# Kernel tuning notes

Measured on AMD Instinct MI355X. Metric: run time of the kernel, lower is better.

## Reference

```python
import jax, jax.numpy as jnp
import numpy as np

S = 60            # voxel grid side
N = 100000        # active voxels
M_PAD = 60000     # padded pairs per kernel offset
C_IN = 64
C_OUT = 64
KV = 27           # kernel volume (3^3)
CENTER = 13


def _build_maps():
    rng = np.random.default_rng(0)
    lin = rng.choice(S ** 3, size=N, replace=False)
    coords = np.stack(np.unravel_index(lin, (S, S, S)), axis=1).astype(np.int64)  # [N,3]
    lut = -np.ones(S ** 3, dtype=np.int64)
    lut[lin] = np.arange(N)
    imap = -np.ones((KV - 1, M_PAD), dtype=np.int32)
    omap = -np.ones((KV - 1, M_PAD), dtype=np.int32)
    row = 0
    for k in range(KV):
        if k == CENTER:
            continue
        d = np.array([k // 9 - 1, (k // 3) % 3 - 1, k % 3 - 1])
        nb = coords + d
        valid = np.all((nb >= 0) & (nb < S), axis=1)
        linnb = nb[:, 0] * S * S + nb[:, 1] * S + nb[:, 2]
        j = np.where(valid, lut[np.clip(linnb, 0, S ** 3 - 1)], -1)
        mask = j >= 0
        src = np.nonzero(mask)[0].astype(np.int32)   # input idx (gather)
        dst = j[mask].astype(np.int32)               # output idx (scatter)
        m = min(src.shape[0], M_PAD)
        imap[row, :m] = src[:m]
        omap[row, :m] = dst[:m]
        row += 1
    return imap, omap


def setup_inputs() -> dict:
    key = jax.random.key(0)
    kf, kw = jax.random.split(key)
    feats = jax.random.normal(kf, (N, C_IN), dtype=jnp.float32)
    stdv = 1.0 / np.sqrt(C_OUT * KV)
    kernel = jax.random.uniform(kw, (KV, C_IN, C_OUT), dtype=jnp.float32,
                                minval=-stdv, maxval=stdv)
    imap_np, omap_np = _build_maps()
    return {
        "feats": feats,
        "kernel": kernel,
        "imap": jnp.asarray(imap_np),
        "omap": jnp.asarray(omap_np),
    }


def reference(feats, kernel, imap, omap):
    # Submanifold sparse 3D conv: center weight applied densely,
    # 26 neighbor offsets via gather -> per-offset GEMM -> scatter-add.
    # feats: [N, Cin], kernel: [27, Cin, Cout], imap/omap: [26, M] (-1 = pad)
    koff = jnp.concatenate([jnp.arange(CENTER), jnp.arange(CENTER + 1, KV)])
    w_off = kernel[koff]                                   # [26, Cin, Cout]
    out = feats @ kernel[CENTER]                           # [N, Cout] center GEMM
    valid = (imap >= 0)                                    # [26, M]
    gathered = feats[jnp.clip(imap, 0)] * valid[..., None].astype(feats.dtype)  # [26, M, Cin]
    partial = jnp.einsum('kmc,kco->kmo', gathered, w_off)  # [26, M, Cout]
    dst = jnp.where(valid, omap, 0).reshape(-1)            # padded rows contribute zeros
    out = out.at[dst].add(partial.reshape(-1, partial.shape[-1]))
    return out
```

## Files before the change

### kernel.cpp

```cpp
#include <hip/hip_runtime.h>


#define N_PTS 100000
#define MPAD  60000
#define C     64
#define NSL   27

typedef short bf16x8 __attribute__((ext_vector_type(8)));
typedef float f32x4  __attribute__((ext_vector_type(4)));

static __device__ inline unsigned short f2bf(float x) {
    unsigned int u = __float_as_uint(x);
    u += 0x7fffu + ((u >> 16) & 1u);
    return (unsigned short)(u >> 16);
}

#define FEATS16_BYTES ((size_t)(N_PTS + 1) * C * 2)
#define WFRAG_OFF     (((FEATS16_BYTES) + 255) & ~(size_t)255)
#define WFRAG_BYTES   ((size_t)NSL * 8192)
#define NBR_OFF       (WFRAG_OFF + WFRAG_BYTES)
#define NBR_BYTES     ((size_t)26 * N_PTS * 4)

#define FEAT_ITEMS 800008
#define WF_ITEMS   (NSL * 2 * 4 * 64)
#define SCAT_ITEMS (26 * MPAD / 4)
#define PREP_TOTAL (FEAT_ITEMS + WF_ITEMS + SCAT_ITEMS)

__global__ __launch_bounds__(256) void prep_one(const float* __restrict__ feats,
                                                const float* __restrict__ kern,
                                                const int* __restrict__ imap,
                                                const int* __restrict__ omap,
                                                unsigned short* __restrict__ f16,
                                                unsigned short* __restrict__ wf,
                                                int* __restrict__ nbr) {
    const int idx = blockIdx.x * 256 + threadIdx.x;
    if (idx < FEAT_ITEMS) {
        bf16x8* dst = (bf16x8*)f16;
        if (idx < FEAT_ITEMS - 8) {
            const float4* src = (const float4*)feats;
            const float4 a = src[2 * idx];
            const float4 b = src[2 * idx + 1];
            bf16x8 v;
            v[0] = (short)f2bf(a.x); v[1] = (short)f2bf(a.y);
            v[2] = (short)f2bf(a.z); v[3] = (short)f2bf(a.w);
            v[4] = (short)f2bf(b.x); v[5] = (short)f2bf(b.y);
            v[6] = (short)f2bf(b.z); v[7] = (short)f2bf(b.w);
            dst[idx] = v;
        } else {
            dst[idx] = (bf16x8){0, 0, 0, 0, 0, 0, 0, 0};
        }
    } else if (idx < FEAT_ITEMS + WF_ITEMS) {
        const int w = idx - FEAT_ITEMS;
        const int lane = w & 63;
        const int rest = w >> 6;
        const int ct = rest & 3;
        const int kk = (rest >> 2) & 1;
        const int s  = rest >> 3;
        bf16x8 v = (bf16x8){0, 0, 0, 0, 0, 0, 0, 0};
        if (s < NSL) {
            const int q = lane >> 4, t = lane & 15;
            const int ksrc = (s == 26) ? 13 : (s + (s >= 13 ? 1 : 0));
            const int k0 = kk * 32 + q * 8;
            const int n  = ct * 16 + t;
            const float* wp = kern + (size_t)ksrc * 4096 + n;
            #pragma unroll
            for (int j = 0; j < 8; ++j) v[j] = (short)f2bf(wp[(size_t)(k0 + j) * 64]);
        }
        ((bf16x8*)wf)[w] = v;
    } else {
        const int k = idx - (FEAT_ITEMS + WF_ITEMS);
        if (k < SCAT_ITEMS) {
            const int s = k / (MPAD / 4);
            const int v = k - s * (MPAD / 4);
            const int4 iv = ((const int4*)(imap + (size_t)s * MPAD))[v];
            const int4 ov = ((const int4*)(omap + (size_t)s * MPAD))[v];
            int* nb = nbr + (size_t)s * N_PTS;
            if (iv.x >= 0) nb[ov.x] = iv.x;
            if (iv.y >= 0) nb[ov.y] = iv.y;
            if (iv.z >= 0) nb[ov.z] = iv.z;
            if (iv.w >= 0) nb[ov.w] = iv.w;
        }
    }
}

static __device__ inline void gl_lds(const char* g, char* l) {
    __builtin_amdgcn_global_load_lds(
        (const __attribute__((address_space(1))) unsigned int*)g,
        (__attribute__((address_space(3))) unsigned int*)l, 16, 0, 0);
}

#define WAITV(n) asm volatile("s_waitcnt vmcnt(" #n ")" ::: "memory")
#define FENCE    asm volatile("" ::: "memory")

__global__ __launch_bounds__(256, 4) void spconv_main(const unsigned short* __restrict__ f16,
                                                      const unsigned short* __restrict__ wf,
                                                      const int* __restrict__ nbr,
                                                      float* __restrict__ out) {
    __shared__ __align__(16) char bsm[3][8192];

    const int lane = threadIdx.x & 63;
    const int wave = threadIdx.x >> 6;
    const int q = lane >> 4, t = lane & 15;
    const int R0 = blockIdx.x * 64 + wave * 16;
    const int row = R0 + t;
    const bool inb = (row < N_PTS);
    const int safe = inb ? row : 0;

    const bf16x8* fv = (const bf16x8*)f16;
    const char* wfb  = (const char*)wf;

    int jr[3];
    bf16x8 Ar[3][2];

#define LOADJ(s_)  do { jr[(s_) % 3] = nbr[(size_t)(s_) * N_PTS + safe]; } while (0)

#define GATHER(s_) do { \
        int j_ = ((s_) == 26) ? (inb ? row : -1) : (inb ? jr[(s_) % 3] : -1); \
        const int jz = ((unsigned)j_ < (unsigned)N_PTS) ? j_ : N_PTS; \
        const bf16x8* ap = fv + (size_t)jz * 8; \
        Ar[(s_) % 3][0] = ap[q]; \
        Ar[(s_) % 3][1] = ap[4 + q]; \
    } while (0)

#define STAGEB(s_) do { \
        const char* gs = wfb + (size_t)(s_) * 8192 + wave * 2048 + lane * 16; \
        char* bd = (char*)bsm[(s_) % 3] + wave * 2048; \
        gl_lds(gs, bd); gl_lds(gs + 1024, bd + 1024); \
    } while (0)

    LOADJ(0); LOADJ(1); FENCE;
    STAGEB(0); FENCE; GATHER(0); FENCE; LOADJ(2); FENCE;
    STAGEB(1); FENCE; GATHER(1); FENCE; LOADJ(3); FENCE;
    WAITV(8);
    __builtin_amdgcn_s_barrier();
    FENCE;

    f32x4 acc[4];
    #pragma unroll
    for (int c = 0; c < 4; ++c) acc[c] = (f32x4){0.f, 0.f, 0.f, 0.f};

    #pragma unroll
    for (int s = 0; s < NSL; ++s) {
        if (s + 2 <= 26) { STAGEB(s + 2); FENCE; GATHER(s + 2); FENCE; }
        if (s + 4 <= 25) { LOADJ(s + 4); FENCE; }

        const char* bb = (const char*)bsm[s % 3];
        bf16x8 B0[4], B1[4];
        #pragma unroll
        for (int ct = 0; ct < 4; ++ct) {
            B0[ct] = *(const bf16x8*)(bb +        ct * 1024 + lane * 16);
            B1[ct] = *(const bf16x8*)(bb + 4096 + ct * 1024 + lane * 16);
        }
        __builtin_amdgcn_s_setprio(1);
        #pragma unroll
        for (int ct = 0; ct < 4; ++ct)
            acc[ct] = __builtin_amdgcn_mfma_f32_16x16x32_bf16(Ar[s % 3][0], B0[ct], acc[ct], 0, 0, 0);
        #pragma unroll
        for (int ct = 0; ct < 4; ++ct)
            acc[ct] = __builtin_amdgcn_mfma_f32_16x16x32_bf16(Ar[s % 3][1], B1[ct], acc[ct], 0, 0, 0);
        __builtin_amdgcn_s_setprio(0);

        if (s < 26) {
            if (s <= 21)      WAITV(8);
            else if (s == 22) WAITV(7);
            else if (s <= 24) WAITV(6);
            else              WAITV(2);
            __builtin_amdgcn_s_barrier();
            FENCE;
        }
    }

#undef LOADJ
#undef GATHER
#undef STAGEB

    #pragma unroll
    for (int i = 0; i < 4; ++i) {
        const int r = R0 + 4 * q + i;
        if (r < N_PTS) {
            #pragma unroll
            for (int ct = 0; ct < 4; ++ct)
                out[(size_t)r * C + ct * 16 + t] = acc[ct][i];
        }
    }
}

extern "C" void kernel_launch(void* const* d_in, const int* in_sizes, int n_in,
                              void* d_out, int out_size, void* d_ws, size_t ws_size,
                              hipStream_t stream) {
    const float* feats = (const float*)d_in[0];
    const float* kern  = (const float*)d_in[1];
    const int*   imap  = (const int*)d_in[2];
    const int*   omap  = (const int*)d_in[3];

    char* ws = (char*)d_ws;
    unsigned short* f16 = (unsigned short*)ws;
    unsigned short* wfr = (unsigned short*)(ws + WFRAG_OFF);
    int*            nbr = (int*)(ws + NBR_OFF);

    prep_one<<<dim3((PREP_TOTAL + 255) / 256), dim3(256), 0, stream>>>(
        feats, kern, imap, omap, f16, wfr, nbr);
    spconv_main<<<dim3((N_PTS + 63) / 64), dim3(256), 0, stream>>>(
        f16, wfr, nbr, (float*)d_out);
}
```

Before: 144.7 us.

## Stream gathered feature rows into LDS via global_load_lds and preload neighbor indices

The A-operand gather for each of the 27 offset slices now goes straight from global memory into a per-wave triple-buffered LDS ring using global_load_lds, instead of into register buffers. All 26 neighbor indices are loaded into registers up front rather than rolled through a small pipeline. The vmcnt wait schedule is simplified to match. The aim is to cut VGPR pressure and make the gather asynchronous like the B staging. In exchange, LDS per block doubles, an extra LDS read is added per slice, 26 index registers are held, and launch bounds drop from 4 to 3 blocks per CU.

```diff
diff --git a/kernel.cpp b/kernel.cpp
--- a/kernel.cpp
+++ b/kernel.cpp
@@ -92,11 +92,12 @@
 #define WAITV(n) asm volatile("s_waitcnt vmcnt(" #n ")" ::: "memory")
 #define FENCE    asm volatile("" ::: "memory")
 
-__global__ __launch_bounds__(256, 4) void spconv_main(const unsigned short* __restrict__ f16,
+__global__ __launch_bounds__(256, 3) void spconv_main(const unsigned short* __restrict__ f16,
                                                       const unsigned short* __restrict__ wf,
                                                       const int* __restrict__ nbr,
                                                       float* __restrict__ out) {
     __shared__ __align__(16) char bsm[3][8192];
+    __shared__ __align__(16) char apool[4][3][2048];
 
     const int lane = threadIdx.x & 63;
     const int wave = threadIdx.x >> 6;
@@ -108,18 +109,19 @@
 
     const bf16x8* fv = (const bf16x8*)f16;
     const char* wfb  = (const char*)wf;
-
-    int jr[3];
-    bf16x8 Ar[3][2];
-
-#define LOADJ(s_)  do { jr[(s_) % 3] = nbr[(size_t)(s_) * N_PTS + safe]; } while (0)
+    char* arng = (char*)apool[wave];
+
+    int jr[26];
+    #pragma unroll
+    for (int s = 0; s < 26; ++s) jr[s] = nbr[(size_t)s * N_PTS + safe];
 
 #define GATHER(s_) do { \
-        int j_ = ((s_) == 26) ? (inb ? row : -1) : (inb ? jr[(s_) % 3] : -1); \
+        int j_ = ((s_) == 26) ? (inb ? row : -1) : (inb ? jr[(s_)] : -1); \
         const int jz = ((unsigned)j_ < (unsigned)N_PTS) ? j_ : N_PTS; \
-        const bf16x8* ap = fv + (size_t)jz * 8; \
-        Ar[(s_) % 3][0] = ap[q]; \
-        Ar[(s_) % 3][1] = ap[4 + q]; \
+        const char* g = (const char*)(fv + (size_t)jz * 8) + q * 16; \
+        char* db = arng + ((s_) % 3) * 2048; \
+        gl_lds(g,      db);        \
+        gl_lds(g + 64, db + 1024); \
     } while (0)
 
 #define STAGEB(s_) do { \
@@ -128,10 +130,9 @@
         gl_lds(gs, bd); gl_lds(gs + 1024, bd + 1024); \
     } while (0)
 
-    LOADJ(0); LOADJ(1); FENCE;
-    STAGEB(0); FENCE; GATHER(0); FENCE; LOADJ(2); FENCE;
-    STAGEB(1); FENCE; GATHER(1); FENCE; LOADJ(3); FENCE;
-    WAITV(8);
+    STAGEB(0); FENCE; GATHER(0); FENCE;
+    STAGEB(1); FENCE; GATHER(1); FENCE;
+    WAITV(4);
     __builtin_amdgcn_s_barrier();
     FENCE;
 
@@ -142,8 +143,10 @@
     #pragma unroll
     for (int s = 0; s < NSL; ++s) {
         if (s + 2 <= 26) { STAGEB(s + 2); FENCE; GATHER(s + 2); FENCE; }
-        if (s + 4 <= 25) { LOADJ(s + 4); FENCE; }
-
+
+        const char* ab = arng + (s % 3) * 2048;
+        const bf16x8 A0 = *(const bf16x8*)(ab +        lane * 16);
+        const bf16x8 A1 = *(const bf16x8*)(ab + 1024 + lane * 16);
         const char* bb = (const char*)bsm[s % 3];
         bf16x8 B0[4], B1[4];
         #pragma unroll
@@ -154,23 +157,20 @@
         __builtin_amdgcn_s_setprio(1);
         #pragma unroll
         for (int ct = 0; ct < 4; ++ct)
-            acc[ct] = __builtin_amdgcn_mfma_f32_16x16x32_bf16(Ar[s % 3][0], B0[ct], acc[ct], 0, 0, 0);
+            acc[ct] = __builtin_amdgcn_mfma_f32_16x16x32_bf16(A0, B0[ct], acc[ct], 0, 0, 0);
         #pragma unroll
         for (int ct = 0; ct < 4; ++ct)
-            acc[ct] = __builtin_amdgcn_mfma_f32_16x16x32_bf16(Ar[s % 3][1], B1[ct], acc[ct], 0, 0, 0);
+            acc[ct] = __builtin_amdgcn_mfma_f32_16x16x32_bf16(A1, B1[ct], acc[ct], 0, 0, 0);
         __builtin_amdgcn_s_setprio(0);
 
         if (s < 26) {
-            if (s <= 21)      WAITV(8);
-            else if (s == 22) WAITV(7);
-            else if (s <= 24) WAITV(6);
-            else              WAITV(2);
+            if (s <= 24) WAITV(4);
+            else         WAITV(0);
             __builtin_amdgcn_s_barrier();
             FENCE;
         }
     }
 
-#undef LOADJ
 #undef GATHER
 #undef STAGEB
 
```

Result: slower. 159.0 us (+9.9%).
